# Optimization experiments

Hardware: AMD Instinct MI355X
Metric: run time of the kernel (lower is better)

## Reference

```python
import jax, jax.numpy as jnp
import numpy as np

IC, HC, L, T, BS = 512, 512, 2, 512, 64
FORGET_BIAS = 1.0


def setup_inputs() -> dict:
    key = jax.random.key(0)
    k_x, k0, k1 = jax.random.split(key, 3)
    # xavier_normal std = sqrt(2/(fan_in+fan_out)), bias zeros (per module init)
    std0 = float(np.sqrt(2.0 / ((IC + HC) + 4 * HC)))
    std1 = float(np.sqrt(2.0 / ((HC + HC) + 4 * HC)))
    return {
        "x": jax.random.normal(k_x, (T, BS, IC), dtype=jnp.float32),
        "W0": jax.random.normal(k0, (IC + HC, 4 * HC), dtype=jnp.float32) * std0,
        "b0": jnp.zeros((4 * HC,), dtype=jnp.float32),
        "W1": jax.random.normal(k1, (HC + HC, 4 * HC), dtype=jnp.float32) * std1,
        "b1": jnp.zeros((4 * HC,), dtype=jnp.float32),
        "h0": jnp.zeros((L, 1, HC), dtype=jnp.float32),
        "c0": jnp.zeros((L, 1, HC), dtype=jnp.float32),
    }


def _run_layer(W, b, x_seq, h_init, c_init):
    def step(carry, xt):
        h, c = carry
        z = jnp.concatenate([xt, h], axis=1) @ W + b  # [bs, 4*hc]
        f, i, o, g = jnp.split(z, 4, axis=1)
        f = jax.nn.sigmoid(f + FORGET_BIAS)
        i = jax.nn.sigmoid(i)
        o = jax.nn.sigmoid(o)
        g = jnp.tanh(g)
        c = c * f + g * i
        h = o * jnp.tanh(c)
        return (h, c), h

    (hT, cT), hs = jax.lax.scan(step, (h_init, c_init), x_seq)
    return hs, hT, cT


def reference(x, W0, b0, W1, b1, h0, c0):
    bs = x.shape[1]
    h = jnp.broadcast_to(h0, (L, bs, HC))
    c = jnp.broadcast_to(c0, (L, bs, HC))
    params = [(W0, b0), (W1, b1)]
    lstm_input = x
    hs_final, cs_final = [], []
    for layer in range(L):
        W, b = params[layer]
        lstm_input, hT, cT = _run_layer(W, b, lstm_input, h[layer], c[layer])
        hs_final.append(hT)
        cs_final.append(cT)
    out = lstm_input  # [T, bs, hc]
    hs = jnp.stack(hs_final, axis=0)  # [L, bs, hc]
    cs = jnp.stack(cs_final, axis=0)
    return (out, (hs, cs))
```

## Files before the change

### kernel.cpp

```cpp
#include <hip/hip_runtime.h>
#include <cstdint>
#include <cstddef>


#define T_STEPS 512
#define WROW 1032
#define CAN64 0x7FC07FC07FC07FC0ULL

typedef float f32x4 __attribute__((ext_vector_type(4)));
typedef short s16x8 __attribute__((ext_vector_type(8)));

__device__ __forceinline__ unsigned short f2bf(float f) {
    unsigned int u = __builtin_bit_cast(unsigned int, f);
    u += 0x7FFFu + ((u >> 16) & 1u);
    return (unsigned short)(u >> 16);
}
__device__ __forceinline__ float sig_(float x)  { return 1.0f / (1.0f + __expf(-x)); }
__device__ __forceinline__ float tanh_(float x) { return 1.0f - 2.0f / (__expf(2.0f * x) + 1.0f); }

__device__ __forceinline__ unsigned long long ld8(const unsigned short* p) {
    return __hip_atomic_load((unsigned long long*)p, __ATOMIC_RELAXED, __HIP_MEMORY_SCOPE_AGENT);
}
__device__ __forceinline__ void stc(unsigned short* p, s16x8 v) {
    ulonglong2 u = __builtin_bit_cast(ulonglong2, v);
    __hip_atomic_store((unsigned long long*)p,     u.x, __ATOMIC_RELAXED, __HIP_MEMORY_SCOPE_AGENT);
    __hip_atomic_store((unsigned long long*)p + 1, u.y, __ATOMIC_RELAXED, __HIP_MEMORY_SCOPE_AGENT);
}


__global__ void k_conv_bf16(const float* __restrict__ src, unsigned short* __restrict__ dst) {
    int i = (blockIdx.x * 256 + threadIdx.x) * 8;
    float4 a = *(const float4*)(src + i);
    float4 b = *(const float4*)(src + i + 4);
    s16x8 o;
    o[0]=(short)f2bf(a.x); o[1]=(short)f2bf(a.y); o[2]=(short)f2bf(a.z); o[3]=(short)f2bf(a.w);
    o[4]=(short)f2bf(b.x); o[5]=(short)f2bf(b.y); o[6]=(short)f2bf(b.z); o[7]=(short)f2bf(b.w);
    *(s16x8*)(dst + i) = o;
}

__global__ void k_transpose_w(const float* __restrict__ W0, const float* __restrict__ W1,
                              unsigned short* __restrict__ WT0, unsigned short* __restrict__ WT1) {
    __shared__ unsigned short tile[32][33];
    const float* W = blockIdx.z ? W1 : W0;
    unsigned short* WT = blockIdx.z ? WT1 : WT0;
    int n0 = blockIdx.x * 32, k0 = blockIdx.y * 32;
    int tx = threadIdx.x, ty = threadIdx.y;
    #pragma unroll
    for (int i = 0; i < 4; i++)
        tile[ty + i*8][tx] = f2bf(W[(size_t)(k0 + ty + i*8) * 2048 + n0 + tx]);
    __syncthreads();
    #pragma unroll
    for (int i = 0; i < 4; i++)
        WT[(size_t)(n0 + ty + i*8) * 1024 + k0 + tx] = tile[tx][ty + i*8];
}

__global__ void k_hinit(const float* __restrict__ h0, unsigned short* __restrict__ hi0,
                        unsigned short* __restrict__ hi1) {
    int idx = blockIdx.x * 256 + threadIdx.x;
    int layer = idx >> 15;
    int r = idx & 32767;
    int b = r >> 9;
    int j = r & 511;
    unsigned short v = f2bf(h0[layer * 512 + j]);
    unsigned short* d = layer ? hi1 : hi0;
    d[(size_t)((j >> 3) * 64 + b) * 8 + (j & 7)] = v;
}

__global__ void k_fill_canary(unsigned long long* __restrict__ dst) {
    size_t i = ((size_t)blockIdx.x * 256 + threadIdx.x) * 2;
    dst[i]     = CAN64;
    dst[i + 1] = CAN64;
}

__global__ __launch_bounds__(256, 1) void k_lstm_fused5(
    const unsigned short* __restrict__ xb,
    const unsigned short* __restrict__ hi0, const unsigned short* __restrict__ hi1,
    const unsigned short* __restrict__ WT0, const unsigned short* __restrict__ WT1,
    const float* __restrict__ b0, const float* __restrict__ b1,
    const float* __restrict__ c0,
    unsigned short* __restrict__ h0s, unsigned short* __restrict__ h1s,
    float* __restrict__ out, float* __restrict__ hs, float* __restrict__ cs)
{
    __shared__ unsigned short Wl[32][WROW];
    __shared__ unsigned short hst[64][8];

    const int isl1 = (int)(blockIdx.x >> 6);
    const int wg   = (int)(blockIdx.x & 63);
    const int tid  = (int)threadIdx.x;
    const int j0   = wg * 8;

    {
        const unsigned short* WT = isl1 ? WT1 : WT0;
        #pragma unroll
        for (int it = 0; it < 16; it++) {
            int idx = it * 256 + tid;
            int row = idx >> 7;
            int ch  = idx & 127;
            int gate = (row >> 4) * 2 + ((row & 15) >> 3);
            int gr = gate * 512 + j0 + (row & 7);
            *(s16x8*)(&Wl[row][ch * 8]) = *(const s16x8*)(WT + (size_t)gr * 1024 + ch * 8);
        }
    }
    __syncthreads();

    const int lane = tid & 63;
    const int wv   = tid >> 6;
    const int q    = lane >> 4;
    const int cc   = lane & 15;
    const int arow = wv * 16 + cc;
    const int jj   = j0 + (cc & 7);
    const int bb   = wv * 16 + q * 4;

    const float* bias = isl1 ? b1 : b0;
    const float bt0 = (cc < 8) ? bias[jj] : bias[512 + jj];
    const float bt1 = (cc < 8) ? bias[1024 + jj] : bias[1536 + jj];
    float cst[4];
    { float ci = c0[isl1 * 512 + jj]; cst[0]=cst[1]=cst[2]=cst[3]=ci; }

    if (!isl1) {
        for (int t = 0; t < T_STEPS; t++) {
            s16x8 ax[16];
            {
                const unsigned short* xp = xb + (size_t)(t * 64 + arow) * 512 + q * 8;
                #pragma unroll
                for (int kk = 0; kk < 16; kk++)
                    ax[kk] = *(const s16x8*)(xp + kk * 32);
            }

            s16x8 ah[16];
            const unsigned short* hb = t ? (h0s + (size_t)(t - 1) * 32768) : hi0;
            bool ok = true;
            #pragma unroll
            for (int kk = 0; kk < 16; kk++) {
                const unsigned short* p = hb + ((size_t)(kk * 4 + q) * 64 + arow) * 8;
                unsigned long long lo = ld8(p), hi = ld8(p + 4);
                ok = ok & (lo != CAN64) & (hi != CAN64);
                ulonglong2 u; u.x = lo; u.y = hi;
                ah[kk] = __builtin_bit_cast(s16x8, u);
            }

            f32x4 a0  = {bt0, bt0, bt0, bt0};
            f32x4 a1  = {bt1, bt1, bt1, bt1};
            f32x4 a0b = {0.f, 0.f, 0.f, 0.f};
            f32x4 a1b = {0.f, 0.f, 0.f, 0.f};
            #pragma unroll
            for (int kk = 0; kk < 16; kk += 2) {
                s16x8 w00 = *(const s16x8*)(&Wl[cc][kk * 32 + q * 8]);
                s16x8 w10 = *(const s16x8*)(&Wl[16 + cc][kk * 32 + q * 8]);
                a0  = __builtin_amdgcn_mfma_f32_16x16x32_bf16(ax[kk], w00, a0, 0, 0, 0);
                a1  = __builtin_amdgcn_mfma_f32_16x16x32_bf16(ax[kk], w10, a1, 0, 0, 0);
                s16x8 w01 = *(const s16x8*)(&Wl[cc][(kk + 1) * 32 + q * 8]);
                s16x8 w11 = *(const s16x8*)(&Wl[16 + cc][(kk + 1) * 32 + q * 8]);
                a0b = __builtin_amdgcn_mfma_f32_16x16x32_bf16(ax[kk + 1], w01, a0b, 0, 0, 0);
                a1b = __builtin_amdgcn_mfma_f32_16x16x32_bf16(ax[kk + 1], w11, a1b, 0, 0, 0);
            }

            while (!ok) {
                __builtin_amdgcn_s_sleep(1);
                ok = true;
                #pragma unroll
                for (int kk = 0; kk < 16; kk++) {
                    const unsigned short* p = hb + ((size_t)(kk * 4 + q) * 64 + arow) * 8;
                    unsigned long long lo = ld8(p), hi = ld8(p + 4);
                    ok = ok & (lo != CAN64) & (hi != CAN64);
                    ulonglong2 u; u.x = lo; u.y = hi;
                    ah[kk] = __builtin_bit_cast(s16x8, u);
                }
            }

            #pragma unroll
            for (int kk = 0; kk < 16; kk += 2) {
                s16x8 w00 = *(const s16x8*)(&Wl[cc][(16 + kk) * 32 + q * 8]);
                s16x8 w10 = *(const s16x8*)(&Wl[16 + cc][(16 + kk) * 32 + q * 8]);
                a0  = __builtin_amdgcn_mfma_f32_16x16x32_bf16(ah[kk], w00, a0, 0, 0, 0);
                a1  = __builtin_amdgcn_mfma_f32_16x16x32_bf16(ah[kk], w10, a1, 0, 0, 0);
                s16x8 w01 = *(const s16x8*)(&Wl[cc][(17 + kk) * 32 + q * 8]);
                s16x8 w11 = *(const s16x8*)(&Wl[16 + cc][(17 + kk) * 32 + q * 8]);
                a0b = __builtin_amdgcn_mfma_f32_16x16x32_bf16(ah[kk + 1], w01, a0b, 0, 0, 0);
                a1b = __builtin_amdgcn_mfma_f32_16x16x32_bf16(ah[kk + 1], w11, a1b, 0, 0, 0);
            }
            a0 = a0 + a0b;
            a1 = a1 + a1b;

            #pragma unroll
            for (int r = 0; r < 4; r++) {
                float z0 = a0[r], z1 = a1[r];
                float p0 = __shfl_xor(z0, 8, 64);
                float p1 = __shfl_xor(z1, 8, 64);
                float zf = (cc < 8) ? z0 : p0;
                float zi = (cc < 8) ? p0 : z0;
                float zo = (cc < 8) ? z1 : p1;
                float zg = (cc < 8) ? p1 : z1;
                float fg = sig_(zf + 1.0f);
                float ig = sig_(zi);
                float og = sig_(zo);
                float gg = tanh_(zg);
                float cn = cst[r] * fg + gg * ig;
                cst[r] = cn;
                float hv = og * tanh_(cn);
                int b = bb + r;
                if (cc < 8) hst[b][cc] = f2bf(hv);
                if (t == T_STEPS - 1) {
                    if (cc < 8) hs[(size_t)b * 512 + jj] = hv;
                    else        cs[(size_t)b * 512 + jj] = cn;
                }
            }

            if (lane < 16) {
                int row = wv * 16 + lane;
                stc(h0s + (size_t)t * 32768 + (size_t)wg * 512 + (size_t)row * 8,
                    *(const s16x8*)(&hst[row][0]));
            }
        }
    } else {
        for (int t = 0; t < T_STEPS; t++) {
            s16x8 ah1[16];
            const unsigned short* hb1 = t ? (h1s + (size_t)(t - 1) * 32768) : hi1;
            bool ok1 = true;
            #pragma unroll
            for (int kk = 0; kk < 16; kk++) {
                const unsigned short* p = hb1 + ((size_t)(kk * 4 + q) * 64 + arow) * 8;
                unsigned long long lo = ld8(p), hi = ld8(p + 4);
                ok1 = ok1 & (lo != CAN64) & (hi != CAN64);
                ulonglong2 u; u.x = lo; u.y = hi;
                ah1[kk] = __builtin_bit_cast(s16x8, u);
            }
            while (!ok1) {
                __builtin_amdgcn_s_sleep(1);
                ok1 = true;
                #pragma unroll
                for (int kk = 0; kk < 16; kk++) {
                    const unsigned short* p = hb1 + ((size_t)(kk * 4 + q) * 64 + arow) * 8;
                    unsigned long long lo = ld8(p), hi = ld8(p + 4);
                    ok1 = ok1 & (lo != CAN64) & (hi != CAN64);
                    ulonglong2 u; u.x = lo; u.y = hi;
                    ah1[kk] = __builtin_bit_cast(s16x8, u);
                }
            }

            s16x8 ah0[16];
            const unsigned short* hb0 = h0s + (size_t)t * 32768;
            bool ok0 = true;
            #pragma unroll
            for (int kk = 0; kk < 16; kk++) {
                const unsigned short* p = hb0 + ((size_t)(kk * 4 + q) * 64 + arow) * 8;
                unsigned long long lo = ld8(p), hi = ld8(p + 4);
                ok0 = ok0 & (lo != CAN64) & (hi != CAN64);
                ulonglong2 u; u.x = lo; u.y = hi;
                ah0[kk] = __builtin_bit_cast(s16x8, u);
            }

            f32x4 a0  = {bt0, bt0, bt0, bt0};
            f32x4 a1  = {bt1, bt1, bt1, bt1};
            f32x4 a0b = {0.f, 0.f, 0.f, 0.f};
            f32x4 a1b = {0.f, 0.f, 0.f, 0.f};
            #pragma unroll
            for (int kk = 0; kk < 16; kk += 2) {
                s16x8 w00 = *(const s16x8*)(&Wl[cc][(16 + kk) * 32 + q * 8]);
                s16x8 w10 = *(const s16x8*)(&Wl[16 + cc][(16 + kk) * 32 + q * 8]);
                a0  = __builtin_amdgcn_mfma_f32_16x16x32_bf16(ah1[kk], w00, a0, 0, 0, 0);
                a1  = __builtin_amdgcn_mfma_f32_16x16x32_bf16(ah1[kk], w10, a1, 0, 0, 0);
                s16x8 w01 = *(const s16x8*)(&Wl[cc][(17 + kk) * 32 + q * 8]);
                s16x8 w11 = *(const s16x8*)(&Wl[16 + cc][(17 + kk) * 32 + q * 8]);
                a0b = __builtin_amdgcn_mfma_f32_16x16x32_bf16(ah1[kk + 1], w01, a0b, 0, 0, 0);
                a1b = __builtin_amdgcn_mfma_f32_16x16x32_bf16(ah1[kk + 1], w11, a1b, 0, 0, 0);
            }

            while (!ok0) {
                __builtin_amdgcn_s_sleep(1);
                ok0 = true;
                #pragma unroll
                for (int kk = 0; kk < 16; kk++) {
                    const unsigned short* p = hb0 + ((size_t)(kk * 4 + q) * 64 + arow) * 8;
                    unsigned long long lo = ld8(p), hi = ld8(p + 4);
                    ok0 = ok0 & (lo != CAN64) & (hi != CAN64);
                    ulonglong2 u; u.x = lo; u.y = hi;
                    ah0[kk] = __builtin_bit_cast(s16x8, u);
                }
            }

            #pragma unroll
            for (int kk = 0; kk < 16; kk += 2) {
                s16x8 w00 = *(const s16x8*)(&Wl[cc][kk * 32 + q * 8]);
                s16x8 w10 = *(const s16x8*)(&Wl[16 + cc][kk * 32 + q * 8]);
                a0  = __builtin_amdgcn_mfma_f32_16x16x32_bf16(ah0[kk], w00, a0, 0, 0, 0);
                a1  = __builtin_amdgcn_mfma_f32_16x16x32_bf16(ah0[kk], w10, a1, 0, 0, 0);
                s16x8 w01 = *(const s16x8*)(&Wl[cc][(kk + 1) * 32 + q * 8]);
                s16x8 w11 = *(const s16x8*)(&Wl[16 + cc][(kk + 1) * 32 + q * 8]);
                a0b = __builtin_amdgcn_mfma_f32_16x16x32_bf16(ah0[kk + 1], w01, a0b, 0, 0, 0);
                a1b = __builtin_amdgcn_mfma_f32_16x16x32_bf16(ah0[kk + 1], w11, a1b, 0, 0, 0);
            }
            a0 = a0 + a0b;
            a1 = a1 + a1b;

            float ov[4];
            #pragma unroll
            for (int r = 0; r < 4; r++) {
                float z0 = a0[r], z1 = a1[r];
                float p0 = __shfl_xor(z0, 8, 64);
                float p1 = __shfl_xor(z1, 8, 64);
                float zf = (cc < 8) ? z0 : p0;
                float zi = (cc < 8) ? p0 : z0;
                float zo = (cc < 8) ? z1 : p1;
                float zg = (cc < 8) ? p1 : z1;
                float fg = sig_(zf + 1.0f);
                float ig = sig_(zi);
                float og = sig_(zo);
                float gg = tanh_(zg);
                float cn = cst[r] * fg + gg * ig;
                cst[r] = cn;
                float hv = og * tanh_(cn);
                ov[r] = hv;
                int b = bb + r;
                if (cc < 8) hst[b][cc] = f2bf(hv);
                if (t == T_STEPS - 1) {
                    if (cc < 8) hs[(size_t)(64 + b) * 512 + jj] = hv;
                    else        cs[(size_t)(64 + b) * 512 + jj] = cn;
                }
            }

            if (lane < 16) {
                int row = wv * 16 + lane;
                stc(h1s + (size_t)t * 32768 + (size_t)wg * 512 + (size_t)row * 8,
                    *(const s16x8*)(&hst[row][0]));
            }

            if (cc >= 8) {
                #pragma unroll
                for (int r = 0; r < 4; r++)
                    out[((size_t)(t * 64 + bb + r)) * 512 + jj] = ov[r];
            }
        }
    }
}


extern "C" void kernel_launch(void* const* d_in, const int* in_sizes, int n_in,
                              void* d_out, int out_size, void* d_ws, size_t ws_size,
                              hipStream_t stream) {
    const float* x  = (const float*)d_in[0];
    const float* W0 = (const float*)d_in[1];
    const float* b0 = (const float*)d_in[2];
    const float* W1 = (const float*)d_in[3];
    const float* b1 = (const float*)d_in[4];
    const float* h0 = (const float*)d_in[5];
    const float* c0 = (const float*)d_in[6];
    float* out = (float*)d_out;

    char* ws = (char*)d_ws;
    unsigned short* xb  = (unsigned short*)(ws);
    unsigned short* h0s = (unsigned short*)(ws + 33554432);
    unsigned short* h1s = (unsigned short*)(ws + 2 * 33554432);
    unsigned short* WT0 = (unsigned short*)(ws + 3 * 33554432);
    unsigned short* WT1 = (unsigned short*)(ws + 3 * 33554432 + 4194304);
    unsigned short* hi0 = (unsigned short*)(ws + 3 * 33554432 + 2 * 4194304);
    unsigned short* hi1 = (unsigned short*)(ws + 3 * 33554432 + 2 * 4194304 + 65536);

    k_fill_canary<<<16384, 256, 0, stream>>>((unsigned long long*)h0s);
    k_conv_bf16<<<8192, 256, 0, stream>>>(x, xb);
    k_transpose_w<<<dim3(64, 32, 2), dim3(32, 8), 0, stream>>>(W0, W1, WT0, WT1);
    k_hinit<<<256, 256, 0, stream>>>(h0, hi0, hi1);

    float* hs = out + 16777216;
    float* cs = hs + 65536;
    k_lstm_fused5<<<128, 256, 0, stream>>>(xb, hi0, hi1, WT0, WT1, b0, b1, c0,
                                           h0s, h1s, out, hs, cs);
}
```

Before: 2.810 ms.

## Split LSTM across batch halves with per-XCD flag-synchronized ring buffer

The persistent LSTM kernel now splits each layer into two batch halves, giving four independent recurrences. It uses 128 active workgroups placed so that all workgroups of a recurrence share one XCD, each computing 16 hidden units with all four gates. When placement is verified via the XCC_ID register, hidden state is exchanged through a small 4-slot ring buffer with sc0 loads and stores and per-wave step flags. This replaces canary polling on the full history buffer, aiming to cut cross-die synchronization latency per timestep. Canary polling remains as a fallback, at the cost of extra flag traffic and reliance on the hardware placing blocks round-robin across XCDs.

```diff
diff --git a/kernel.cpp b/kernel.cpp
--- a/kernel.cpp
+++ b/kernel.cpp
@@ -6,9 +6,12 @@
 #define T_STEPS 512
 #define WROW 1032
 #define CAN64 0x7FC07FC07FC07FC0ULL
+#define POLL_BOUND 4096
+#define PLC_BOUND  (1 << 20)
 
 typedef float f32x4 __attribute__((ext_vector_type(4)));
 typedef short s16x8 __attribute__((ext_vector_type(8)));
+typedef unsigned int u32x4 __attribute__((ext_vector_type(4)));
 
 __device__ __forceinline__ unsigned short f2bf(float f) {
     unsigned int u = __builtin_bit_cast(unsigned int, f);
@@ -26,6 +29,15 @@
     __hip_atomic_store((unsigned long long*)p,     u.x, __ATOMIC_RELAXED, __HIP_MEMORY_SCOPE_AGENT);
     __hip_atomic_store((unsigned long long*)p + 1, u.y, __ATOMIC_RELAXED, __HIP_MEMORY_SCOPE_AGENT);
 }
+
+__device__ __forceinline__ void ld16_sc0(s16x8* d_, const unsigned short* p) {
+    asm volatile("global_load_dwordx4 %0, %1, off sc0" : "=v"(*d_) : "v"(p));
+}
+__device__ __forceinline__ void st16_sc0(unsigned short* p, s16x8 v) {
+    asm volatile("global_store_dwordx4 %0, %1, off sc0" :: "v"(p), "v"(v) : "memory");
+}
+#define VMCNT0() do { asm volatile("s_waitcnt vmcnt(0)" ::: "memory"); \
+                      __builtin_amdgcn_sched_barrier(0); } while (0)
 
 
 __global__ void k_conv_bf16(const float* __restrict__ src, unsigned short* __restrict__ dst) {
@@ -54,281 +66,280 @@
         WT[(size_t)(n0 + ty + i*8) * 1024 + k0 + tx] = tile[tx][ty + i*8];
 }
 
-__global__ void k_hinit(const float* __restrict__ h0, unsigned short* __restrict__ hi0,
-                        unsigned short* __restrict__ hi1) {
-    int idx = blockIdx.x * 256 + threadIdx.x;
-    int layer = idx >> 15;
-    int r = idx & 32767;
-    int b = r >> 9;
-    int j = r & 511;
-    unsigned short v = f2bf(h0[layer * 512 + j]);
-    unsigned short* d = layer ? hi1 : hi0;
-    d[(size_t)((j >> 3) * 64 + b) * 8 + (j & 7)] = v;
-}
-
 __global__ void k_fill_canary(unsigned long long* __restrict__ dst) {
     size_t i = ((size_t)blockIdx.x * 256 + threadIdx.x) * 2;
-    dst[i]     = CAN64;
-    dst[i + 1] = CAN64;
-}
-
-__global__ __launch_bounds__(256, 1) void k_lstm_fused5(
+    dst[i] = CAN64; dst[i + 1] = CAN64;
+}
+
+__global__ void k_hinit2(const float* __restrict__ h0, unsigned short* __restrict__ ring) {
+    int idx = blockIdx.x * 256 + threadIdx.x;
+    int d = idx >> 14;
+    int r = idx & 16383;
+    int jb = r >> 8;
+    int e = r & 7;
+    ring[(size_t)(d * 4 + 3) * 16384 + r] = f2bf(h0[(d >> 1) * 512 + jb * 8 + e]);
+}
+
+__global__ __launch_bounds__(256, 1) void k_lstm_fused7(
     const unsigned short* __restrict__ xb,
-    const unsigned short* __restrict__ hi0, const unsigned short* __restrict__ hi1,
     const unsigned short* __restrict__ WT0, const unsigned short* __restrict__ WT1,
     const float* __restrict__ b0, const float* __restrict__ b1,
     const float* __restrict__ c0,
-    unsigned short* __restrict__ h0s, unsigned short* __restrict__ h1s,
+    unsigned short* __restrict__ h0m, unsigned short* __restrict__ h1m,
+    unsigned short* __restrict__ ring, unsigned int* __restrict__ flags,
+    unsigned int* __restrict__ plc,
     float* __restrict__ out, float* __restrict__ hs, float* __restrict__ cs)
 {
-    __shared__ unsigned short Wl[32][WROW];
-    __shared__ unsigned short hst[64][8];
-
-    const int isl1 = (int)(blockIdx.x >> 6);
-    const int wg   = (int)(blockIdx.x & 63);
-    const int tid  = (int)threadIdx.x;
-    const int j0   = wg * 8;
+    __shared__ unsigned short Wl[64][WROW];
+    __shared__ unsigned short hst[32][16];
+
+    const int d = (int)(blockIdx.x & 7);
+    if (d >= 4) return;
+    const int wid = (int)(blockIdx.x >> 3);
+    const int tid = (int)threadIdx.x;
+    const int layer = d >> 1;
+    const int bt    = d & 1;
+    const int j0    = wid * 16;
 
     {
-        const unsigned short* WT = isl1 ? WT1 : WT0;
+        const unsigned short* WT = layer ? WT1 : WT0;
         #pragma unroll
-        for (int it = 0; it < 16; it++) {
+        for (int it = 0; it < 32; it++) {
             int idx = it * 256 + tid;
             int row = idx >> 7;
             int ch  = idx & 127;
-            int gate = (row >> 4) * 2 + ((row & 15) >> 3);
-            int gr = gate * 512 + j0 + (row & 7);
-            *(s16x8*)(&Wl[row][ch * 8]) = *(const s16x8*)(WT + (size_t)gr * 1024 + ch * 8);
+            int gate = row >> 4, jl = row & 15;
+            *(s16x8*)(&Wl[row][ch * 8]) =
+                *(const s16x8*)(WT + (size_t)(gate * 512 + j0 + jl) * 1024 + ch * 8);
         }
     }
     __syncthreads();
 
     const int lane = tid & 63;
     const int wv   = tid >> 6;
+    const int mh   = wv >> 1;
+    const int jo   = wv & 1;
     const int q    = lane >> 4;
     const int cc   = lane & 15;
-    const int arow = wv * 16 + cc;
-    const int jj   = j0 + (cc & 7);
-    const int bb   = wv * 16 + q * 4;
-
-    const float* bias = isl1 ? b1 : b0;
+    const int jj   = j0 + jo * 8 + (cc & 7);
+    const int w0row = ((cc < 8) ? 0 : 16) + jo * 8 + (cc & 7);
+    const int w1row = w0row + 32;
+
+    const float* bias = layer ? b1 : b0;
     const float bt0 = (cc < 8) ? bias[jj] : bias[512 + jj];
     const float bt1 = (cc < 8) ? bias[1024 + jj] : bias[1536 + jj];
     float cst[4];
-    { float ci = c0[isl1 * 512 + jj]; cst[0]=cst[1]=cst[2]=cst[3]=ci; }
-
-    if (!isl1) {
-        for (int t = 0; t < T_STEPS; t++) {
-            s16x8 ax[16];
-            {
-                const unsigned short* xp = xb + (size_t)(t * 64 + arow) * 512 + q * 8;
-                #pragma unroll
-                for (int kk = 0; kk < 16; kk++)
-                    ax[kk] = *(const s16x8*)(xp + kk * 32);
-            }
-
-            s16x8 ah[16];
-            const unsigned short* hb = t ? (h0s + (size_t)(t - 1) * 32768) : hi0;
-            bool ok = true;
+    { float ci = c0[layer * 512 + jj]; cst[0]=cst[1]=cst[2]=cst[3]=ci; }
+
+    unsigned int* myf = flags + (size_t)(d * 32 + wid) * 4 + wv;
+    unsigned short* hmL = layer ? h1m : h0m;
+    unsigned short* ringd = ring + (size_t)d * 4 * 16384;
+
+    unsigned myxcd;
+    asm volatile("s_getreg_b32 %0, hwreg(HW_REG_XCC_ID)" : "=s"(myxcd));
+    if (tid == 0)
+        __hip_atomic_store(plc + d * 32 + wid, myxcd + 1u,
+                           __ATOMIC_RELAXED, __HIP_MEMORY_SCOPE_AGENT);
+    bool fastok;
+    {
+        unsigned pv = 1u;
+        int spins = 0; bool got = true;
+        while (true) {
+            if (lane < 32)
+                pv = __hip_atomic_load(plc + d * 32 + lane, __ATOMIC_RELAXED, __HIP_MEMORY_SCOPE_AGENT);
+            if (__ballot(pv == 0u) == 0ull) break;
+            if (++spins > PLC_BOUND) { got = false; break; }
+            __builtin_amdgcn_s_sleep(8);
+        }
+        fastok = got && (__ballot(lane < 32 && pv != myxcd + 1u) == 0ull);
+    }
+
+    for (int t = 0; t < T_STEPS; t++) {
+        f32x4 a0  = {bt0, bt0, bt0, bt0};
+        f32x4 a1  = {bt1, bt1, bt1, bt1};
+        f32x4 a0b = {0.f, 0.f, 0.f, 0.f};
+        f32x4 a1b = {0.f, 0.f, 0.f, 0.f};
+        s16x8 afr[16];
+        s16x8 axh[16];
+        const size_t frch[1] = {0};  (void)frch;
+
+        if (t == 0) {
+            const unsigned short* rp = ringd + (size_t)3 * 16384;
             #pragma unroll
             for (int kk = 0; kk < 16; kk++) {
-                const unsigned short* p = hb + ((size_t)(kk * 4 + q) * 64 + arow) * 8;
+                const unsigned short* p = rp + ((size_t)(kk * 4 + q) * 32 + mh * 16 + cc) * 8;
                 unsigned long long lo = ld8(p), hi = ld8(p + 4);
-                ok = ok & (lo != CAN64) & (hi != CAN64);
                 ulonglong2 u; u.x = lo; u.y = hi;
-                ah[kk] = __builtin_bit_cast(s16x8, u);
-            }
-
-            f32x4 a0  = {bt0, bt0, bt0, bt0};
-            f32x4 a1  = {bt1, bt1, bt1, bt1};
-            f32x4 a0b = {0.f, 0.f, 0.f, 0.f};
-            f32x4 a1b = {0.f, 0.f, 0.f, 0.f};
-            #pragma unroll
-            for (int kk = 0; kk < 16; kk += 2) {
-                s16x8 w00 = *(const s16x8*)(&Wl[cc][kk * 32 + q * 8]);
-                s16x8 w10 = *(const s16x8*)(&Wl[16 + cc][kk * 32 + q * 8]);
-                a0  = __builtin_amdgcn_mfma_f32_16x16x32_bf16(ax[kk], w00, a0, 0, 0, 0);
-                a1  = __builtin_amdgcn_mfma_f32_16x16x32_bf16(ax[kk], w10, a1, 0, 0, 0);
-                s16x8 w01 = *(const s16x8*)(&Wl[cc][(kk + 1) * 32 + q * 8]);
-                s16x8 w11 = *(const s16x8*)(&Wl[16 + cc][(kk + 1) * 32 + q * 8]);
-                a0b = __builtin_amdgcn_mfma_f32_16x16x32_bf16(ax[kk + 1], w01, a0b, 0, 0, 0);
-                a1b = __builtin_amdgcn_mfma_f32_16x16x32_bf16(ax[kk + 1], w11, a1b, 0, 0, 0);
-            }
-
-            while (!ok) {
-                __builtin_amdgcn_s_sleep(1);
-                ok = true;
+                afr[kk] = __builtin_bit_cast(s16x8, u);
+            }
+        } else {
+            bool have = false;
+            if (fastok) {
+                const unsigned int* fp = flags + (size_t)(d * 32 + (lane & 31)) * 4;
+                int spins = 0; bool okp = true;
+                while (true) {
+                    u32x4 fv;
+                    asm volatile("global_load_dwordx4 %0, %1, off sc0" : "=v"(fv) : "v"(fp));
+                    asm volatile("s_waitcnt vmcnt(0)" ::: "memory");
+                    __builtin_amdgcn_sched_barrier(0);
+                    unsigned m0 = fv[0] < fv[1] ? fv[0] : fv[1];
+                    unsigned m1 = fv[2] < fv[3] ? fv[2] : fv[3];
+                    unsigned m  = m0 < m1 ? m0 : m1;
+                    if (__ballot(m < (unsigned)t) == 0ull) break;
+                    if (++spins > POLL_BOUND) { okp = false; break; }
+                    __builtin_amdgcn_s_sleep(1);
+                }
+                if (okp) {
+                    const unsigned short* rp = ringd + (size_t)((t + 3) & 3) * 16384;
+                    #pragma unroll
+                    for (int kk = 0; kk < 16; kk++)
+                        ld16_sc0(&afr[kk], rp + ((size_t)(kk * 4 + q) * 32 + mh * 16 + cc) * 8);
+                    VMCNT0();
+                    have = true;
+                } else {
+                    fastok = false;
+                }
+            }
+            if (!have) {
+                const unsigned short* hb = hmL + ((size_t)(t - 1) * 2 + bt) * 16384;
+                bool ok = true;
                 #pragma unroll
                 for (int kk = 0; kk < 16; kk++) {
-                    const unsigned short* p = hb + ((size_t)(kk * 4 + q) * 64 + arow) * 8;
+                    const unsigned short* p = hb + ((size_t)(kk * 4 + q) * 32 + mh * 16 + cc) * 8;
                     unsigned long long lo = ld8(p), hi = ld8(p + 4);
                     ok = ok & (lo != CAN64) & (hi != CAN64);
                     ulonglong2 u; u.x = lo; u.y = hi;
-                    ah[kk] = __builtin_bit_cast(s16x8, u);
-                }
-            }
-
-            #pragma unroll
-            for (int kk = 0; kk < 16; kk += 2) {
-                s16x8 w00 = *(const s16x8*)(&Wl[cc][(16 + kk) * 32 + q * 8]);
-                s16x8 w10 = *(const s16x8*)(&Wl[16 + cc][(16 + kk) * 32 + q * 8]);
-                a0  = __builtin_amdgcn_mfma_f32_16x16x32_bf16(ah[kk], w00, a0, 0, 0, 0);
-                a1  = __builtin_amdgcn_mfma_f32_16x16x32_bf16(ah[kk], w10, a1, 0, 0, 0);
-                s16x8 w01 = *(const s16x8*)(&Wl[cc][(17 + kk) * 32 + q * 8]);
-                s16x8 w11 = *(const s16x8*)(&Wl[16 + cc][(17 + kk) * 32 + q * 8]);
-                a0b = __builtin_amdgcn_mfma_f32_16x16x32_bf16(ah[kk + 1], w01, a0b, 0, 0, 0);
-                a1b = __builtin_amdgcn_mfma_f32_16x16x32_bf16(ah[kk + 1], w11, a1b, 0, 0, 0);
-            }
-            a0 = a0 + a0b;
-            a1 = a1 + a1b;
-
-            #pragma unroll
-            for (int r = 0; r < 4; r++) {
-                float z0 = a0[r], z1 = a1[r];
-                float p0 = __shfl_xor(z0, 8, 64);
-                float p1 = __shfl_xor(z1, 8, 64);
-                float zf = (cc < 8) ? z0 : p0;
-                float zi = (cc < 8) ? p0 : z0;
-                float zo = (cc < 8) ? z1 : p1;
-                float zg = (cc < 8) ? p1 : z1;
-                float fg = sig_(zf + 1.0f);
-                float ig = sig_(zi);
-                float og = sig_(zo);
-                float gg = tanh_(zg);
-                float cn = cst[r] * fg + gg * ig;
-                cst[r] = cn;
-                float hv = og * tanh_(cn);
-                int b = bb + r;
-                if (cc < 8) hst[b][cc] = f2bf(hv);
-                if (t == T_STEPS - 1) {
-                    if (cc < 8) hs[(size_t)b * 512 + jj] = hv;
-                    else        cs[(size_t)b * 512 + jj] = cn;
-                }
-            }
-
-            if (lane < 16) {
-                int row = wv * 16 + lane;
-                stc(h0s + (size_t)t * 32768 + (size_t)wg * 512 + (size_t)row * 8,
-                    *(const s16x8*)(&hst[row][0]));
-            }
-        }
-    } else {
-        for (int t = 0; t < T_STEPS; t++) {
-            s16x8 ah1[16];
-            const unsigned short* hb1 = t ? (h1s + (size_t)(t - 1) * 32768) : hi1;
-            bool ok1 = true;
+                    afr[kk] = __builtin_bit_cast(s16x8, u);
+                }
+                while (!ok) {
+                    __builtin_amdgcn_s_sleep(1);
+                    ok = true;
+                    #pragma unroll
+                    for (int kk = 0; kk < 16; kk++) {
+                        const unsigned short* p = hb + ((size_t)(kk * 4 + q) * 32 + mh * 16 + cc) * 8;
+                        unsigned long long lo = ld8(p), hi = ld8(p + 4);
+                        ok = ok & (lo != CAN64) & (hi != CAN64);
+                        ulonglong2 u; u.x = lo; u.y = hi;
+                        afr[kk] = __builtin_bit_cast(s16x8, u);
+                    }
+                }
+            }
+        }
+
+        if (layer == 0) {
+            const unsigned short* xp = xb + (size_t)(t * 64 + bt * 32 + mh * 16 + cc) * 512 + q * 8;
+            #pragma unroll
+            for (int kk = 0; kk < 16; kk++)
+                axh[kk] = *(const s16x8*)(xp + kk * 32);
+        } else {
+            const unsigned short* hp = h0m + ((size_t)t * 2 + bt) * 16384;
+            bool ok0 = true;
             #pragma unroll
             for (int kk = 0; kk < 16; kk++) {
-                const unsigned short* p = hb1 + ((size_t)(kk * 4 + q) * 64 + arow) * 8;
-                unsigned long long lo = ld8(p), hi = ld8(p + 4);
-                ok1 = ok1 & (lo != CAN64) & (hi != CAN64);
-                ulonglong2 u; u.x = lo; u.y = hi;
-                ah1[kk] = __builtin_bit_cast(s16x8, u);
-            }
-            while (!ok1) {
-                __builtin_amdgcn_s_sleep(1);
-                ok1 = true;
-                #pragma unroll
-                for (int kk = 0; kk < 16; kk++) {
-                    const unsigned short* p = hb1 + ((size_t)(kk * 4 + q) * 64 + arow) * 8;
-                    unsigned long long lo = ld8(p), hi = ld8(p + 4);
-                    ok1 = ok1 & (lo != CAN64) & (hi != CAN64);
-                    ulonglong2 u; u.x = lo; u.y = hi;
-                    ah1[kk] = __builtin_bit_cast(s16x8, u);
-                }
-            }
-
-            s16x8 ah0[16];
-            const unsigned short* hb0 = h0s + (size_t)t * 32768;
-            bool ok0 = true;
-            #pragma unroll
-            for (int kk = 0; kk < 16; kk++) {
-                const unsigned short* p = hb0 + ((size_t)(kk * 4 + q) * 64 + arow) * 8;
+                const unsigned short* p = hp + ((size_t)(kk * 4 + q) * 32 + mh * 16 + cc) * 8;
                 unsigned long long lo = ld8(p), hi = ld8(p + 4);
                 ok0 = ok0 & (lo != CAN64) & (hi != CAN64);
                 ulonglong2 u; u.x = lo; u.y = hi;
-                ah0[kk] = __builtin_bit_cast(s16x8, u);
-            }
-
-            f32x4 a0  = {bt0, bt0, bt0, bt0};
-            f32x4 a1  = {bt1, bt1, bt1, bt1};
-            f32x4 a0b = {0.f, 0.f, 0.f, 0.f};
-            f32x4 a1b = {0.f, 0.f, 0.f, 0.f};
+                axh[kk] = __builtin_bit_cast(s16x8, u);
+            }
             #pragma unroll
             for (int kk = 0; kk < 16; kk += 2) {
-                s16x8 w00 = *(const s16x8*)(&Wl[cc][(16 + kk) * 32 + q * 8]);
-                s16x8 w10 = *(const s16x8*)(&Wl[16 + cc][(16 + kk) * 32 + q * 8]);
-                a0  = __builtin_amdgcn_mfma_f32_16x16x32_bf16(ah1[kk], w00, a0, 0, 0, 0);
-                a1  = __builtin_amdgcn_mfma_f32_16x16x32_bf16(ah1[kk], w10, a1, 0, 0, 0);
-                s16x8 w01 = *(const s16x8*)(&Wl[cc][(17 + kk) * 32 + q * 8]);
-                s16x8 w11 = *(const s16x8*)(&Wl[16 + cc][(17 + kk) * 32 + q * 8]);
-                a0b = __builtin_amdgcn_mfma_f32_16x16x32_bf16(ah1[kk + 1], w01, a0b, 0, 0, 0);
-                a1b = __builtin_amdgcn_mfma_f32_16x16x32_bf16(ah1[kk + 1], w11, a1b, 0, 0, 0);
-            }
-
+                s16x8 w00 = *(const s16x8*)(&Wl[w0row][512 + kk * 32 + q * 8]);
+                s16x8 w10 = *(const s16x8*)(&Wl[w1row][512 + kk * 32 + q * 8]);
+                a0  = __builtin_amdgcn_mfma_f32_16x16x32_bf16(afr[kk], w00, a0, 0, 0, 0);
+                a1  = __builtin_amdgcn_mfma_f32_16x16x32_bf16(afr[kk], w10, a1, 0, 0, 0);
+                s16x8 w01 = *(const s16x8*)(&Wl[w0row][512 + (kk + 1) * 32 + q * 8]);
+                s16x8 w11 = *(const s16x8*)(&Wl[w1row][512 + (kk + 1) * 32 + q * 8]);
+                a0b = __builtin_amdgcn_mfma_f32_16x16x32_bf16(afr[kk + 1], w01, a0b, 0, 0, 0);
+                a1b = __builtin_amdgcn_mfma_f32_16x16x32_bf16(afr[kk + 1], w11, a1b, 0, 0, 0);
+            }
             while (!ok0) {
                 __builtin_amdgcn_s_sleep(1);
                 ok0 = true;
                 #pragma unroll
                 for (int kk = 0; kk < 16; kk++) {
-                    const unsigned short* p = hb0 + ((size_t)(kk * 4 + q) * 64 + arow) * 8;
+                    const unsigned short* p = hp + ((size_t)(kk * 4 + q) * 32 + mh * 16 + cc) * 8;
                     unsigned long long lo = ld8(p), hi = ld8(p + 4);
                     ok0 = ok0 & (lo != CAN64) & (hi != CAN64);
                     ulonglong2 u; u.x = lo; u.y = hi;
-                    ah0[kk] = __builtin_bit_cast(s16x8, u);
-                }
-            }
-
+                    axh[kk] = __builtin_bit_cast(s16x8, u);
+                }
+            }
+        }
+
+        #pragma unroll
+        for (int kk = 0; kk < 16; kk += 2) {
+            s16x8 w00 = *(const s16x8*)(&Wl[w0row][kk * 32 + q * 8]);
+            s16x8 w10 = *(const s16x8*)(&Wl[w1row][kk * 32 + q * 8]);
+            a0  = __builtin_amdgcn_mfma_f32_16x16x32_bf16(axh[kk], w00, a0, 0, 0, 0);
+            a1  = __builtin_amdgcn_mfma_f32_16x16x32_bf16(axh[kk], w10, a1, 0, 0, 0);
+            s16x8 w01 = *(const s16x8*)(&Wl[w0row][(kk + 1) * 32 + q * 8]);
+            s16x8 w11 = *(const s16x8*)(&Wl[w1row][(kk + 1) * 32 + q * 8]);
+            a0b = __builtin_amdgcn_mfma_f32_16x16x32_bf16(axh[kk + 1], w01, a0b, 0, 0, 0);
+            a1b = __builtin_amdgcn_mfma_f32_16x16x32_bf16(axh[kk + 1], w11, a1b, 0, 0, 0);
+        }
+        if (layer == 0) {
             #pragma unroll
             for (int kk = 0; kk < 16; kk += 2) {
-                s16x8 w00 = *(const s16x8*)(&Wl[cc][kk * 32 + q * 8]);
-                s16x8 w10 = *(const s16x8*)(&Wl[16 + cc][kk * 32 + q * 8]);
-                a0  = __builtin_amdgcn_mfma_f32_16x16x32_bf16(ah0[kk], w00, a0, 0, 0, 0);
-                a1  = __builtin_amdgcn_mfma_f32_16x16x32_bf16(ah0[kk], w10, a1, 0, 0, 0);
-                s16x8 w01 = *(const s16x8*)(&Wl[cc][(kk + 1) * 32 + q * 8]);
-                s16x8 w11 = *(const s16x8*)(&Wl[16 + cc][(kk + 1) * 32 + q * 8]);
-                a0b = __builtin_amdgcn_mfma_f32_16x16x32_bf16(ah0[kk + 1], w01, a0b, 0, 0, 0);
-                a1b = __builtin_amdgcn_mfma_f32_16x16x32_bf16(ah0[kk + 1], w11, a1b, 0, 0, 0);
-            }
-            a0 = a0 + a0b;
-            a1 = a1 + a1b;
-
-            float ov[4];
+                s16x8 w00 = *(const s16x8*)(&Wl[w0row][512 + kk * 32 + q * 8]);
+                s16x8 w10 = *(const s16x8*)(&Wl[w1row][512 + kk * 32 + q * 8]);
+                a0  = __builtin_amdgcn_mfma_f32_16x16x32_bf16(afr[kk], w00, a0, 0, 0, 0);
+                a1  = __builtin_amdgcn_mfma_f32_16x16x32_bf16(afr[kk], w10, a1, 0, 0, 0);
+                s16x8 w01 = *(const s16x8*)(&Wl[w0row][512 + (kk + 1) * 32 + q * 8]);
+                s16x8 w11 = *(const s16x8*)(&Wl[w1row][512 + (kk + 1) * 32 + q * 8]);
+                a0b = __builtin_amdgcn_mfma_f32_16x16x32_bf16(afr[kk + 1], w01, a0b, 0, 0, 0);
+                a1b = __builtin_amdgcn_mfma_f32_16x16x32_bf16(afr[kk + 1], w11, a1b, 0, 0, 0);
+            }
+        }
+
+        a0 = a0 + a0b;
+        a1 = a1 + a1b;
+        float hvr[4], cnr[4];
+        #pragma unroll
+        for (int r = 0; r < 4; r++) {
+            float z0 = a0[r], z1 = a1[r];
+            float p0 = __shfl_xor(z0, 8, 64);
+            float p1 = __shfl_xor(z1, 8, 64);
+            float zf = (cc < 8) ? z0 : p0;
+            float zi = (cc < 8) ? p0 : z0;
+            float zo = (cc < 8) ? z1 : p1;
+            float zg = (cc < 8) ? p1 : z1;
+            float fg = sig_(zf + 1.0f);
+            float ig = sig_(zi);
+            float og = sig_(zo);
+            float gg = tanh_(zg);
+            float cn = cst[r] * fg + gg * ig;
+            cst[r] = cn;
+            float hv = og * tanh_(cn);
+            hvr[r] = hv; cnr[r] = cn;
+            if (cc < 8) hst[mh * 16 + q * 4 + r][jo * 8 + cc] = f2bf(hv);
+        }
+
+        if (lane < 16) {
+            s16x8 hv16 = *(const s16x8*)(&hst[mh * 16 + lane][jo * 8]);
+            size_t ch = (size_t)((wid * 2 + jo) * 32 + mh * 16 + lane) * 8;
+            st16_sc0(ringd + (size_t)(t & 3) * 16384 + ch, hv16);
+            stc(hmL + ((size_t)t * 2 + bt) * 16384 + ch, hv16);
+        }
+        VMCNT0();
+        if (lane == 0) {
+            unsigned fvv = (unsigned)(t + 1);
+            asm volatile("global_store_dword %0, %1, off sc0" :: "v"(myf), "v"(fvv) : "memory");
+        }
+
+        if (layer == 1 && cc >= 8) {
             #pragma unroll
             for (int r = 0; r < 4; r++) {
-                float z0 = a0[r], z1 = a1[r];
-                float p0 = __shfl_xor(z0, 8, 64);
-                float p1 = __shfl_xor(z1, 8, 64);
-                float zf = (cc < 8) ? z0 : p0;
-                float zi = (cc < 8) ? p0 : z0;
-                float zo = (cc < 8) ? z1 : p1;
-                float zg = (cc < 8) ? p1 : z1;
-                float fg = sig_(zf + 1.0f);
-                float ig = sig_(zi);
-                float og = sig_(zo);
-                float gg = tanh_(zg);
-                float cn = cst[r] * fg + gg * ig;
-                cst[r] = cn;
-                float hv = og * tanh_(cn);
-                ov[r] = hv;
-                int b = bb + r;
-                if (cc < 8) hst[b][cc] = f2bf(hv);
-                if (t == T_STEPS - 1) {
-                    if (cc < 8) hs[(size_t)(64 + b) * 512 + jj] = hv;
-                    else        cs[(size_t)(64 + b) * 512 + jj] = cn;
-                }
-            }
-
-            if (lane < 16) {
-                int row = wv * 16 + lane;
-                stc(h1s + (size_t)t * 32768 + (size_t)wg * 512 + (size_t)row * 8,
-                    *(const s16x8*)(&hst[row][0]));
-            }
-
-            if (cc >= 8) {
-                #pragma unroll
-                for (int r = 0; r < 4; r++)
-                    out[((size_t)(t * 64 + bb + r)) * 512 + jj] = ov[r];
+                int bg = bt * 32 + mh * 16 + q * 4 + r;
+                out[((size_t)t * 64 + bg) * 512 + jj] = hvr[r];
+            }
+        }
+        if (t == T_STEPS - 1) {
+            #pragma unroll
+            for (int r = 0; r < 4; r++) {
+                int bg = bt * 32 + mh * 16 + q * 4 + r;
+                if (cc < 8) hs[((size_t)layer * 64 + bg) * 512 + jj] = hvr[r];
+                else        cs[((size_t)layer * 64 + bg) * 512 + jj] = cnr[r];
             }
         }
     }
@@ -348,21 +359,23 @@
     float* out = (float*)d_out;
 
     char* ws = (char*)d_ws;
-    unsigned short* xb  = (unsigned short*)(ws);
-    unsigned short* h0s = (unsigned short*)(ws + 33554432);
-    unsigned short* h1s = (unsigned short*)(ws + 2 * 33554432);
-    unsigned short* WT0 = (unsigned short*)(ws + 3 * 33554432);
-    unsigned short* WT1 = (unsigned short*)(ws + 3 * 33554432 + 4194304);
-    unsigned short* hi0 = (unsigned short*)(ws + 3 * 33554432 + 2 * 4194304);
-    unsigned short* hi1 = (unsigned short*)(ws + 3 * 33554432 + 2 * 4194304 + 65536);
-
-    k_fill_canary<<<16384, 256, 0, stream>>>((unsigned long long*)h0s);
+    unsigned short* xb   = (unsigned short*)(ws);
+    unsigned short* WT0  = (unsigned short*)(ws + 33554432);
+    unsigned short* WT1  = (unsigned short*)(ws + 37748736);
+    unsigned short* h0m  = (unsigned short*)(ws + 41943040);
+    unsigned short* h1m  = (unsigned short*)(ws + 75497472);
+    unsigned short* ring = (unsigned short*)(ws + 109051904);
+    unsigned int*   flags = (unsigned int*)(ws + 109576192);
+    unsigned int*   plc   = (unsigned int*)(ws + 109578240);
+
+    hipMemsetAsync(flags, 0, 4096, stream);
+    k_fill_canary<<<16384, 256, 0, stream>>>((unsigned long long*)h0m);
     k_conv_bf16<<<8192, 256, 0, stream>>>(x, xb);
     k_transpose_w<<<dim3(64, 32, 2), dim3(32, 8), 0, stream>>>(W0, W1, WT0, WT1);
-    k_hinit<<<256, 256, 0, stream>>>(h0, hi0, hi1);
+    k_hinit2<<<256, 256, 0, stream>>>(h0, ring);
 
     float* hs = out + 16777216;
     float* cs = hs + 65536;
-    k_lstm_fused5<<<128, 256, 0, stream>>>(xb, hi0, hi1, WT0, WT1, b0, b1, c0,
-                                           h0s, h1s, out, hs, cs);
-}
+    k_lstm_fused7<<<256, 256, 0, stream>>>(xb, WT0, WT1, b0, b1, c0,
+                                           h0m, h1m, ring, flags, plc, out, hs, cs);
+}
```

New measurement: 9.468 ms. 3.37x slower.

## Poll recurrent state per chunk and prefetch next-step inputs in LSTM loop

Applied to the files above, without the earlier changes.

Replaces the all-or-nothing canary check on the previous hidden state with a per-chunk spin-wait inside the MFMA loop. Each chunk's matmul can now start as soon as its own slice has arrived instead of waiting for the whole vector. Layer 0 also prefetches the next timestep's x operands while waiting on h, which moves that load off the critical recurrence path. The cost is more register pressure from holding ax across iterations, plus a branchy inner loop that may schedule MFMAs worse.

```diff
diff --git a/kernel.cpp b/kernel.cpp
--- a/kernel.cpp
+++ b/kernel.cpp
@@ -72,7 +72,7 @@
     dst[i + 1] = CAN64;
 }
 
-__global__ __launch_bounds__(256, 1) void k_lstm_fused5(
+__global__ __launch_bounds__(256, 1) void k_lstm_fused8(
     const unsigned short* __restrict__ xb,
     const unsigned short* __restrict__ hi0, const unsigned short* __restrict__ hi1,
     const unsigned short* __restrict__ WT0, const unsigned short* __restrict__ WT1,
@@ -118,24 +118,21 @@
     { float ci = c0[isl1 * 512 + jj]; cst[0]=cst[1]=cst[2]=cst[3]=ci; }
 
     if (!isl1) {
+        s16x8 ax[16];
+        {
+            const unsigned short* xp = xb + (size_t)(0 * 64 + arow) * 512 + q * 8;
+            #pragma unroll
+            for (int kk = 0; kk < 16; kk++)
+                ax[kk] = *(const s16x8*)(xp + kk * 32);
+        }
+
         for (int t = 0; t < T_STEPS; t++) {
-            s16x8 ax[16];
-            {
-                const unsigned short* xp = xb + (size_t)(t * 64 + arow) * 512 + q * 8;
-                #pragma unroll
-                for (int kk = 0; kk < 16; kk++)
-                    ax[kk] = *(const s16x8*)(xp + kk * 32);
-            }
-
             s16x8 ah[16];
             const unsigned short* hb = t ? (h0s + (size_t)(t - 1) * 32768) : hi0;
-            bool ok = true;
             #pragma unroll
             for (int kk = 0; kk < 16; kk++) {
                 const unsigned short* p = hb + ((size_t)(kk * 4 + q) * 64 + arow) * 8;
-                unsigned long long lo = ld8(p), hi = ld8(p + 4);
-                ok = ok & (lo != CAN64) & (hi != CAN64);
-                ulonglong2 u; u.x = lo; u.y = hi;
+                ulonglong2 u; u.x = ld8(p); u.y = ld8(p + 4);
                 ah[kk] = __builtin_bit_cast(s16x8, u);
             }
 
@@ -155,29 +152,32 @@
                 a1b = __builtin_amdgcn_mfma_f32_16x16x32_bf16(ax[kk + 1], w11, a1b, 0, 0, 0);
             }
 
-            while (!ok) {
-                __builtin_amdgcn_s_sleep(1);
-                ok = true;
+            {
+                int tn = (t + 1 < T_STEPS) ? (t + 1) : t;
+                const unsigned short* xp = xb + (size_t)(tn * 64 + arow) * 512 + q * 8;
                 #pragma unroll
-                for (int kk = 0; kk < 16; kk++) {
-                    const unsigned short* p = hb + ((size_t)(kk * 4 + q) * 64 + arow) * 8;
-                    unsigned long long lo = ld8(p), hi = ld8(p + 4);
-                    ok = ok & (lo != CAN64) & (hi != CAN64);
-                    ulonglong2 u; u.x = lo; u.y = hi;
-                    ah[kk] = __builtin_bit_cast(s16x8, u);
-                }
-            }
-
-            #pragma unroll
-            for (int kk = 0; kk < 16; kk += 2) {
+                for (int kk = 0; kk < 16; kk++)
+                    ax[kk] = *(const s16x8*)(xp + kk * 32);
+            }
+
+            #pragma unroll
+            for (int kk = 0; kk < 16; kk++) {
+                const unsigned short* p = hb + ((size_t)(kk * 4 + q) * 64 + arow) * 8;
+                ulonglong2 u = __builtin_bit_cast(ulonglong2, ah[kk]);
+                while ((u.x == CAN64) | (u.y == CAN64)) {
+                    __builtin_amdgcn_s_sleep(1);
+                    u.x = ld8(p); u.y = ld8(p + 4);
+                }
+                s16x8 hf = __builtin_bit_cast(s16x8, u);
                 s16x8 w00 = *(const s16x8*)(&Wl[cc][(16 + kk) * 32 + q * 8]);
                 s16x8 w10 = *(const s16x8*)(&Wl[16 + cc][(16 + kk) * 32 + q * 8]);
-                a0  = __builtin_amdgcn_mfma_f32_16x16x32_bf16(ah[kk], w00, a0, 0, 0, 0);
-                a1  = __builtin_amdgcn_mfma_f32_16x16x32_bf16(ah[kk], w10, a1, 0, 0, 0);
-                s16x8 w01 = *(const s16x8*)(&Wl[cc][(17 + kk) * 32 + q * 8]);
-                s16x8 w11 = *(const s16x8*)(&Wl[16 + cc][(17 + kk) * 32 + q * 8]);
-                a0b = __builtin_amdgcn_mfma_f32_16x16x32_bf16(ah[kk + 1], w01, a0b, 0, 0, 0);
-                a1b = __builtin_amdgcn_mfma_f32_16x16x32_bf16(ah[kk + 1], w11, a1b, 0, 0, 0);
+                if (kk & 1) {
+                    a0b = __builtin_amdgcn_mfma_f32_16x16x32_bf16(hf, w00, a0b, 0, 0, 0);
+                    a1b = __builtin_amdgcn_mfma_f32_16x16x32_bf16(hf, w10, a1b, 0, 0, 0);
+                } else {
+                    a0  = __builtin_amdgcn_mfma_f32_16x16x32_bf16(hf, w00, a0, 0, 0, 0);
+                    a1  = __builtin_amdgcn_mfma_f32_16x16x32_bf16(hf, w10, a1, 0, 0, 0);
+                }
             }
             a0 = a0 + a0b;
             a1 = a1 + a1b;
@@ -205,7 +205,6 @@
                     else        cs[(size_t)b * 512 + jj] = cn;
                 }
             }
-
             if (lane < 16) {
                 int row = wv * 16 + lane;
                 stc(h0s + (size_t)t * 32768 + (size_t)wg * 512 + (size_t)row * 8,
@@ -216,37 +215,18 @@
         for (int t = 0; t < T_STEPS; t++) {
             s16x8 ah1[16];
             const unsigned short* hb1 = t ? (h1s + (size_t)(t - 1) * 32768) : hi1;
-            bool ok1 = true;
             #pragma unroll
             for (int kk = 0; kk < 16; kk++) {
                 const unsigned short* p = hb1 + ((size_t)(kk * 4 + q) * 64 + arow) * 8;
-                unsigned long long lo = ld8(p), hi = ld8(p + 4);
-                ok1 = ok1 & (lo != CAN64) & (hi != CAN64);
-                ulonglong2 u; u.x = lo; u.y = hi;
+                ulonglong2 u; u.x = ld8(p); u.y = ld8(p + 4);
                 ah1[kk] = __builtin_bit_cast(s16x8, u);
             }
-            while (!ok1) {
-                __builtin_amdgcn_s_sleep(1);
-                ok1 = true;
-                #pragma unroll
-                for (int kk = 0; kk < 16; kk++) {
-                    const unsigned short* p = hb1 + ((size_t)(kk * 4 + q) * 64 + arow) * 8;
-                    unsigned long long lo = ld8(p), hi = ld8(p + 4);
-                    ok1 = ok1 & (lo != CAN64) & (hi != CAN64);
-                    ulonglong2 u; u.x = lo; u.y = hi;
-                    ah1[kk] = __builtin_bit_cast(s16x8, u);
-                }
-            }
-
             s16x8 ah0[16];
             const unsigned short* hb0 = h0s + (size_t)t * 32768;
-            bool ok0 = true;
             #pragma unroll
             for (int kk = 0; kk < 16; kk++) {
                 const unsigned short* p = hb0 + ((size_t)(kk * 4 + q) * 64 + arow) * 8;
-                unsigned long long lo = ld8(p), hi = ld8(p + 4);
-                ok0 = ok0 & (lo != CAN64) & (hi != CAN64);
-                ulonglong2 u; u.x = lo; u.y = hi;
+                ulonglong2 u; u.x = ld8(p); u.y = ld8(p + 4);
                 ah0[kk] = __builtin_bit_cast(s16x8, u);
             }
 
@@ -254,41 +234,45 @@
             f32x4 a1  = {bt1, bt1, bt1, bt1};
             f32x4 a0b = {0.f, 0.f, 0.f, 0.f};
             f32x4 a1b = {0.f, 0.f, 0.f, 0.f};
-            #pragma unroll
-            for (int kk = 0; kk < 16; kk += 2) {
+
+            #pragma unroll
+            for (int kk = 0; kk < 16; kk++) {
+                const unsigned short* p = hb1 + ((size_t)(kk * 4 + q) * 64 + arow) * 8;
+                ulonglong2 u = __builtin_bit_cast(ulonglong2, ah1[kk]);
+                while ((u.x == CAN64) | (u.y == CAN64)) {
+                    __builtin_amdgcn_s_sleep(1);
+                    u.x = ld8(p); u.y = ld8(p + 4);
+                }
+                s16x8 hf = __builtin_bit_cast(s16x8, u);
                 s16x8 w00 = *(const s16x8*)(&Wl[cc][(16 + kk) * 32 + q * 8]);
                 s16x8 w10 = *(const s16x8*)(&Wl[16 + cc][(16 + kk) * 32 + q * 8]);
-                a0  = __builtin_amdgcn_mfma_f32_16x16x32_bf16(ah1[kk], w00, a0, 0, 0, 0);
-                a1  = __builtin_amdgcn_mfma_f32_16x16x32_bf16(ah1[kk], w10, a1, 0, 0, 0);
-                s16x8 w01 = *(const s16x8*)(&Wl[cc][(17 + kk) * 32 + q * 8]);
-                s16x8 w11 = *(const s16x8*)(&Wl[16 + cc][(17 + kk) * 32 + q * 8]);
-                a0b = __builtin_amdgcn_mfma_f32_16x16x32_bf16(ah1[kk + 1], w01, a0b, 0, 0, 0);
-                a1b = __builtin_amdgcn_mfma_f32_16x16x32_bf16(ah1[kk + 1], w11, a1b, 0, 0, 0);
-            }
-
-            while (!ok0) {
-                __builtin_amdgcn_s_sleep(1);
-                ok0 = true;
-                #pragma unroll
-                for (int kk = 0; kk < 16; kk++) {
-                    const unsigned short* p = hb0 + ((size_t)(kk * 4 + q) * 64 + arow) * 8;
-                    unsigned long long lo = ld8(p), hi = ld8(p + 4);
-                    ok0 = ok0 & (lo != CAN64) & (hi != CAN64);
-                    ulonglong2 u; u.x = lo; u.y = hi;
-                    ah0[kk] = __builtin_bit_cast(s16x8, u);
-                }
-            }
-
-            #pragma unroll
-            for (int kk = 0; kk < 16; kk += 2) {
+                if (kk & 1) {
+                    a0b = __builtin_amdgcn_mfma_f32_16x16x32_bf16(hf, w00, a0b, 0, 0, 0);
+                    a1b = __builtin_amdgcn_mfma_f32_16x16x32_bf16(hf, w10, a1b, 0, 0, 0);
+                } else {
+                    a0  = __builtin_amdgcn_mfma_f32_16x16x32_bf16(hf, w00, a0, 0, 0, 0);
+                    a1  = __builtin_amdgcn_mfma_f32_16x16x32_bf16(hf, w10, a1, 0, 0, 0);
+                }
+            }
+
+            #pragma unroll
+            for (int kk = 0; kk < 16; kk++) {
+                const unsigned short* p = hb0 + ((size_t)(kk * 4 + q) * 64 + arow) * 8;
+                ulonglong2 u = __builtin_bit_cast(ulonglong2, ah0[kk]);
+                while ((u.x == CAN64) | (u.y == CAN64)) {
+                    __builtin_amdgcn_s_sleep(1);
+                    u.x = ld8(p); u.y = ld8(p + 4);
+                }
+                s16x8 hf = __builtin_bit_cast(s16x8, u);
                 s16x8 w00 = *(const s16x8*)(&Wl[cc][kk * 32 + q * 8]);
                 s16x8 w10 = *(const s16x8*)(&Wl[16 + cc][kk * 32 + q * 8]);
-                a0  = __builtin_amdgcn_mfma_f32_16x16x32_bf16(ah0[kk], w00, a0, 0, 0, 0);
-                a1  = __builtin_amdgcn_mfma_f32_16x16x32_bf16(ah0[kk], w10, a1, 0, 0, 0);
-                s16x8 w01 = *(const s16x8*)(&Wl[cc][(kk + 1) * 32 + q * 8]);
-                s16x8 w11 = *(const s16x8*)(&Wl[16 + cc][(kk + 1) * 32 + q * 8]);
-                a0b = __builtin_amdgcn_mfma_f32_16x16x32_bf16(ah0[kk + 1], w01, a0b, 0, 0, 0);
-                a1b = __builtin_amdgcn_mfma_f32_16x16x32_bf16(ah0[kk + 1], w11, a1b, 0, 0, 0);
+                if (kk & 1) {
+                    a0b = __builtin_amdgcn_mfma_f32_16x16x32_bf16(hf, w00, a0b, 0, 0, 0);
+                    a1b = __builtin_amdgcn_mfma_f32_16x16x32_bf16(hf, w10, a1b, 0, 0, 0);
+                } else {
+                    a0  = __builtin_amdgcn_mfma_f32_16x16x32_bf16(hf, w00, a0, 0, 0, 0);
+                    a1  = __builtin_amdgcn_mfma_f32_16x16x32_bf16(hf, w10, a1, 0, 0, 0);
+                }
             }
             a0 = a0 + a0b;
             a1 = a1 + a1b;
@@ -363,6 +347,6 @@
 
     float* hs = out + 16777216;
     float* cs = hs + 65536;
-    k_lstm_fused5<<<128, 256, 0, stream>>>(xb, hi0, hi1, WT0, WT1, b0, b1, c0,
+    k_lstm_fused8<<<128, 256, 0, stream>>>(xb, hi0, hi1, WT0, WT1, b0, b1, c0,
                                            h0s, h1s, out, hs, cs);
 }
```

New measurement: 4.452 ms. 1.58x slower.
